# Kernel tuning notes

Measured on AMD Instinct MI355X. Metric: run time of the kernel, lower is better.

## Reference

```python
import jax, jax.numpy as jnp
import numpy as np

GRID_SIZE = 5
SPLINE_ORDER = 3
GRID_LO, GRID_HI = -1.0, 1.0
N_COEFF = GRID_SIZE + SPLINE_ORDER  # 8


def make_grid(in_features):
    # (in_features, grid_size + 2*spline_order + 1) = (in, 12)
    h = (GRID_HI - GRID_LO) / GRID_SIZE
    g = jnp.arange(-SPLINE_ORDER, GRID_SIZE + SPLINE_ORDER + 1, dtype=jnp.float32) * h + GRID_LO
    return jnp.broadcast_to(g, (in_features, g.shape[0]))


def b_splines(x, grid):
    # x: (N, in); grid: (in, G). Returns (N, in, grid_size+spline_order).
    xe = x[..., None]
    bases = ((xe >= grid[:, :-1]) & (xe < grid[:, 1:])).astype(x.dtype)
    for k in range(1, SPLINE_ORDER + 1):
        left = (xe - grid[:, :-(k + 1)]) / (grid[:, k:-1] - grid[:, :-(k + 1)]) * bases[..., :-1]
        right = (grid[:, k + 1:] - xe) / (grid[:, k + 1:] - grid[:, 1:-k]) * bases[..., 1:]
        bases = left + right
    return bases


def kan_linear(x, base_w, spline_w, scaler, grid):
    # base branch: SiLU(x) @ base_w^T
    base_out = jax.nn.silu(x) @ base_w.T
    # spline branch: basis (N,in,c) contracted with scaled spline weight (out,in,c)
    b = b_splines(x, grid)
    sw = spline_w * scaler[..., None]
    spline_out = jnp.einsum('nic,oic->no', b, sw)
    return base_out + spline_out


def setup_inputs() -> dict:
    key = jax.random.key(0)
    ks = jax.random.split(key, 7)
    d_model, d_hid = 512, 2049  # d_ff + 1
    s = 0.1  # keep activations roughly inside grid range
    return {
        "x": jax.random.normal(ks[0], (4096, d_model), dtype=jnp.float32) * 0.3,
        "base_w1": jax.random.normal(ks[1], (d_hid, d_model), dtype=jnp.float32) * s,
        "spline_w1": jax.random.normal(ks[2], (d_hid, d_model, N_COEFF), dtype=jnp.float32) * s,
        "scaler1": jax.random.normal(ks[3], (d_hid, d_model), dtype=jnp.float32) * s,
        "base_w2": jax.random.normal(ks[4], (d_model, d_hid), dtype=jnp.float32) * s,
        "spline_w2": jax.random.normal(ks[5], (d_model, d_hid, N_COEFF), dtype=jnp.float32) * s,
        "scaler2": jax.random.normal(ks[6], (d_model, d_hid), dtype=jnp.float32) * s,
    }


def reference(x, base_w1, spline_w1, scaler1, base_w2, spline_w2, scaler2):
    grid1 = make_grid(x.shape[-1])
    h = kan_linear(x, base_w1, spline_w1, scaler1, grid1)
    grid2 = make_grid(h.shape[-1])
    out = kan_linear(h, base_w2, spline_w2, scaler2, grid2)
    return out
```

## Files before the change

kernel.cpp:

```cpp
#include <hip/hip_runtime.h>
#include <hip/hip_bf16.h>

#define T_TOK 4096
#define I1    512
#define O1    2049
#define O1P   2176
#define K1    4608
#define NG1   576
#define I2    2049
#define O2    512
#define K2P   18496
#define NG2   2312
#define HLD   2176
#define SPLITS2 8
#define KLEN2 2368
#define NBY   32
#define PW1_NB 4896
#define E1_NB  9216
#define PW2_NB 8192

typedef __attribute__((ext_vector_type(8))) short short8;
typedef __attribute__((ext_vector_type(4))) float floatx4;
typedef __attribute__((address_space(3))) void* lds_ptr_t;
typedef const __attribute__((address_space(1))) void* gmem_ptr_t;

__device__ __forceinline__ unsigned short f2bf(float f) {
  union { __hip_bfloat16 h; unsigned short u; } cv;
  cv.h = __float2bfloat16(f);
  return cv.u;
}
__device__ __forceinline__ unsigned bfr(float f) {
  union { float f; unsigned u; } c; c.f = f;
  return (c.u + 0x8000u) >> 16;
}
__device__ __forceinline__ float silu_f(float x) { return x / (1.0f + __expf(-x)); }

__device__ __forceinline__ uint4 spline_pack(float h) {
  float u = (h + 2.2f) * 2.5f;
  int ji = (int)u;
  ji = ji < 0 ? 0 : (ji > 10 ? 10 : ji);
  float t = u - (float)ji;
  float it = 1.0f - t, t2 = t * t, t3 = t2 * t;
  float b0 = it * it * it * (1.0f / 6.0f);
  float b1 = (3.0f * t3 - 6.0f * t2 + 4.0f) * (1.0f / 6.0f);
  float b2 = (-3.0f * t3 + 3.0f * t2 + 3.0f * t + 1.0f) * (1.0f / 6.0f);
  float b3 = t3 * (1.0f / 6.0f);
  unsigned pk01 = bfr(b0) | (bfr(b1) << 16);
  unsigned pk23 = bfr(b2) | (bfr(b3) << 16);
  unsigned long long p64 = (unsigned long long)pk01 | ((unsigned long long)pk23 << 32);
  bool inR = (h >= -2.2f) && (h < 2.2f);
  p64 = inR ? p64 : 0ull;
  int sh = (ji - 3) * 16;
  int shr = sh < 0 ? -sh : 0;
  int shl = sh < 0 ? 0 : sh;
  __uint128_t v = ((__uint128_t)(p64 >> shr)) << shl;
  union { __uint128_t q; uint4 u4; } cv;
  cv.q = v;
  return cv.u4;
}

__global__ void prep1_kernel(const float* __restrict__ x, const float* __restrict__ bw1,
                             const float* __restrict__ sw1, const float* __restrict__ sc1,
                             unsigned short* __restrict__ A1, unsigned short* __restrict__ W1) {
  int b = blockIdx.x;
  union { unsigned short s[8]; uint4 v; } pk;
  if (b < PW1_NB) {
    int idx = b * 256 + threadIdx.x;
    int o = idx / NG1, g = idx - o * NG1;
    if (o >= O1) {
      pk.v = make_uint4(0u, 0u, 0u, 0u);
    } else if (g < 512) {
      const float4* p = (const float4*)&sw1[(size_t)o * 4096 + g * 8];
      float4 a = p[0], c = p[1];
      float sc = sc1[(size_t)o * I1 + g];
      pk.s[0] = f2bf(a.x * sc); pk.s[1] = f2bf(a.y * sc);
      pk.s[2] = f2bf(a.z * sc); pk.s[3] = f2bf(a.w * sc);
      pk.s[4] = f2bf(c.x * sc); pk.s[5] = f2bf(c.y * sc);
      pk.s[6] = f2bf(c.z * sc); pk.s[7] = f2bf(c.w * sc);
    } else {
      const float4* p = (const float4*)&bw1[(size_t)o * I1 + (g - 512) * 8];
      float4 a = p[0], c = p[1];
      pk.s[0] = f2bf(a.x); pk.s[1] = f2bf(a.y); pk.s[2] = f2bf(a.z); pk.s[3] = f2bf(a.w);
      pk.s[4] = f2bf(c.x); pk.s[5] = f2bf(c.y); pk.s[6] = f2bf(c.z); pk.s[7] = f2bf(c.w);
    }
    *(uint4*)&W1[(size_t)o * K1 + (size_t)g * 8] = pk.v;
  } else {
    int idx = (b - PW1_NB) * 256 + threadIdx.x;
    int m = idx / NG1, g = idx - m * NG1;
    if (g < 512) {
      pk.v = spline_pack(x[(size_t)m * I1 + g]);
    } else {
      const float4* p = (const float4*)&x[(size_t)m * I1 + (size_t)(g - 512) * 8];
      float4 a = p[0], c = p[1];
      pk.s[0] = f2bf(silu_f(a.x)); pk.s[1] = f2bf(silu_f(a.y));
      pk.s[2] = f2bf(silu_f(a.z)); pk.s[3] = f2bf(silu_f(a.w));
      pk.s[4] = f2bf(silu_f(c.x)); pk.s[5] = f2bf(silu_f(c.y));
      pk.s[6] = f2bf(silu_f(c.z)); pk.s[7] = f2bf(silu_f(c.w));
    }
    *(uint4*)&A1[(size_t)m * K1 + (size_t)g * 8] = pk.v;
  }
}

__global__ void pack_w2_kernel(const float* __restrict__ bw2, const float* __restrict__ sw2,
                               const float* __restrict__ sc2, unsigned short* __restrict__ W2) {
  int idx = blockIdx.x * 256 + threadIdx.x;
  int o = idx >> 12, g = idx & 4095;
  if (g >= NG2) return;
  union { unsigned short s[8]; uint4 v; } pk;
  if (g < 2049) {
    const float4* p = (const float4*)&sw2[(size_t)o * 16392 + (size_t)g * 8];
    float4 a = p[0], c = p[1];
    float sc = sc2[(size_t)o * I2 + g];
    pk.s[0] = f2bf(a.x * sc); pk.s[1] = f2bf(a.y * sc);
    pk.s[2] = f2bf(a.z * sc); pk.s[3] = f2bf(a.w * sc);
    pk.s[4] = f2bf(c.x * sc); pk.s[5] = f2bf(c.y * sc);
    pk.s[6] = f2bf(c.z * sc); pk.s[7] = f2bf(c.w * sc);
  } else if (g < 2306) {
    int c0 = (g - 2049) * 8;
#pragma unroll
    for (int j = 0; j < 8; ++j) {
      int k = c0 + j;
      pk.s[j] = (k < I2) ? f2bf(bw2[(size_t)o * I2 + k]) : (unsigned short)0;
    }
  } else {
    pk.v = make_uint4(0u, 0u, 0u, 0u);
  }
  *(uint4*)&W2[(size_t)o * K2P + (size_t)g * 8] = pk.v;
}

__global__ void expand2_kernel(const float* __restrict__ H, unsigned short* __restrict__ A) {
  int g = blockIdx.x * 256 + threadIdx.x;
  if (g >= NG2) return;
  int m = blockIdx.y;
  uint4 val;
  if (g < 2049) {
    val = spline_pack(H[(size_t)m * HLD + g]);
  } else if (g < 2306) {
    int c0 = (g - 2049) * 8;
    union { unsigned short s[8]; uint4 v; } pk;
#pragma unroll
    for (int c = 0; c < 8; ++c) {
      int idx = c0 + c;
      float v = 0.0f;
      if (idx < I2) v = silu_f(H[(size_t)m * HLD + idx]);
      pk.s[c] = f2bf(v);
    }
    val = pk.v;
  } else {
    val = make_uint4(0u, 0u, 0u, 0u);
  }
  *(uint4*)(A + (size_t)m * K2P + (size_t)g * 8) = val;
}

__global__ __launch_bounds__(256, 4)
void gemm_bt_kernel(const unsigned short* __restrict__ Aw, const unsigned short* __restrict__ Bw,
                    float* __restrict__ C, int Ktot, int N, int ldc, int kLen,
                    int nBx, int storeMode)
{
  __shared__ __align__(16) unsigned short As[128 * 64];
  __shared__ __align__(16) unsigned short Bs[128 * 64];

  const int Lb = blockIdx.x;
  const int m8 = Lb & 7;
  const int r  = Lb >> 3;
  const int bx = r % nBx;
  const int p  = m8 + ((r / nBx) << 3);
  const int by = p & (NBY - 1);
  const int bz = p >> 5;

  const int tid = threadIdx.x;
  const int ks = bz * kLen;
  int ke = ks + kLen; if (ke > Ktot) ke = Ktot;

  const int w = tid >> 6, L = tid & 63, q = L >> 4, ln = L & 15;
  const int wm = (w & 1) << 6, wn = (w >> 1) << 6;

  floatx4 zf = {0.f, 0.f, 0.f, 0.f};
  floatx4 acc[4][4];
#pragma unroll
  for (int mt = 0; mt < 4; ++mt)
#pragma unroll
    for (int nt = 0; nt < 4; ++nt)
      acc[mt][nt] = zf;

  const unsigned short* ga[4];
  const unsigned short* gb[4];
  int ldsOff[4];
#pragma unroll
  for (int r4 = 0; r4 < 4; ++r4) {
    int e = r4 * 256 + tid;
    int br = e >> 3;
    int cg = (e & 7) ^ (br & 7);
    ga[r4] = Aw + ((long)by * 128 + br) * (long)Ktot + ks + cg * 8;
    gb[r4] = Bw + ((long)bx * 128 + br) * (long)Ktot + ks + cg * 8;
    ldsOff[r4] = e * 8;
  }

  for (int kc = ks; kc < ke; kc += 64) {
    __syncthreads();
#pragma unroll
    for (int r4 = 0; r4 < 4; ++r4) {
      __builtin_amdgcn_global_load_lds((gmem_ptr_t)ga[r4], (lds_ptr_t)&As[ldsOff[r4]], 16, 0, 0);
      ga[r4] += 64;
      __builtin_amdgcn_global_load_lds((gmem_ptr_t)gb[r4], (lds_ptr_t)&Bs[ldsOff[r4]], 16, 0, 0);
      gb[r4] += 64;
    }
    __syncthreads();

#pragma unroll
    for (int s = 0; s < 2; ++s) {
      short8 af[4], bf[4];
#pragma unroll
      for (int mt = 0; mt < 4; ++mt) {
        int rr = wm + mt * 16 + ln;
        int cl = ((s << 2) | q) ^ (rr & 7);
        af[mt] = *(const short8*)&As[rr * 64 + cl * 8];
      }
#pragma unroll
      for (int nt = 0; nt < 4; ++nt) {
        int rr = wn + nt * 16 + ln;
        int cl = ((s << 2) | q) ^ (rr & 7);
        bf[nt] = *(const short8*)&Bs[rr * 64 + cl * 8];
      }
#pragma unroll
      for (int mt = 0; mt < 4; ++mt)
#pragma unroll
        for (int nt = 0; nt < 4; ++nt)
          acc[mt][nt] = __builtin_amdgcn_mfma_f32_16x16x32_bf16(af[mt], bf[nt], acc[mt][nt], 0, 0, 0);
    }
  }

  if (storeMode == 0) {
#pragma unroll
    for (int mt = 0; mt < 4; ++mt) {
#pragma unroll
      for (int nt = 0; nt < 4; ++nt) {
        int n = bx * 128 + wn + nt * 16 + ln;
        if (n < N) {
          int m0 = by * 128 + wm + mt * 16 + q * 4;
#pragma unroll
          for (int rg = 0; rg < 4; ++rg)
            C[(size_t)(m0 + rg) * ldc + n] = acc[mt][nt][rg];
        }
      }
    }
  } else {
#pragma unroll
    for (int mt = 0; mt < 4; ++mt) {
#pragma unroll
      for (int nt = 0; nt < 4; ++nt) {
        int n = bx * 128 + wn + nt * 16 + ln;
        if (n < N) {
          int m0 = by * 128 + wm + mt * 16 + q * 4;
#pragma unroll
          for (int rg = 0; rg < 4; ++rg)
            atomicAdd(&C[(size_t)(m0 + rg) * ldc + n], acc[mt][nt][rg]);
        }
      }
    }
  }
}

extern "C" void kernel_launch(void* const* d_in, const int* in_sizes, int n_in,
                              void* d_out, int out_size, void* d_ws, size_t ws_size,
                              hipStream_t stream) {
  const float* x   = (const float*)d_in[0];
  const float* bw1 = (const float*)d_in[1];
  const float* sw1 = (const float*)d_in[2];
  const float* sc1 = (const float*)d_in[3];
  const float* bw2 = (const float*)d_in[4];
  const float* sw2 = (const float*)d_in[5];
  const float* sc2 = (const float*)d_in[6];
  float* out = (float*)d_out;

  float* H = (float*)d_ws;
  unsigned short* A2 = (unsigned short*)(H + (size_t)T_TOK * HLD);
  unsigned short* A1 = A2 + (size_t)T_TOK * K2P;
  unsigned short* W1 = A1 + (size_t)T_TOK * K1;
  unsigned short* W2 = A1;

  hipMemsetAsync(d_out, 0, (size_t)out_size * sizeof(float), stream);

  prep1_kernel<<<PW1_NB + E1_NB, 256, 0, stream>>>(x, bw1, sw1, sc1, A1, W1);

  gemm_bt_kernel<<<(O1P / 128) * NBY, 256, 0, stream>>>(
      A1, W1, H, K1, O1, HLD, K1, O1P / 128, 0);

  pack_w2_kernel<<<PW2_NB, 256, 0, stream>>>(bw2, sw2, sc2, W2);

  expand2_kernel<<<dim3((NG2 + 255) / 256, T_TOK), 256, 0, stream>>>(H, A2);

  gemm_bt_kernel<<<(O2 / 128) * NBY * SPLITS2, 256, 0, stream>>>(
      A2, W2, out, K2P, O2, O2, KLEN2, O2 / 128, 2);
}
```

Baseline: 417.3 us.

## Replace GEMM with 256x128 triple-buffered pipelined kernel and split odd column to GEMV

Replaces the 128x128 double-sync GEMM with a 512-thread, 256x128-tile kernel that triple-buffers LDS, interleaves direct global-to-LDS prefetch with MFMA phases, and raises MFMA wave priority. The odd 2049th output column of layer 1 moves to a separate GEMV kernel so the main GEMM works on an aligned 2048-wide N with no padding tiles. The layer-2 split-K factor drops from 8 to 4, which halves the atomic traffic. The tradeoffs are higher LDS and register pressure, fewer workgroups in flight, and an extra kernel launch.

```diff
diff --git a/kernel.cpp b/kernel.cpp
--- a/kernel.cpp
+++ b/kernel.cpp
@@ -11,10 +11,9 @@
 #define O2    512
 #define K2P   18496
 #define NG2   2312
-#define HLD   2176
-#define SPLITS2 8
-#define KLEN2 2368
-#define NBY   32
+#define N1G   2048
+#define SPLITS2 4
+#define KLEN2 4672
 #define PW1_NB 4896
 #define E1_NB  9216
 #define PW2_NB 8192
@@ -28,6 +27,9 @@
   union { __hip_bfloat16 h; unsigned short u; } cv;
   cv.h = __float2bfloat16(f);
   return cv.u;
+}
+__device__ __forceinline__ float b2f(unsigned short u) {
+  union { float f; unsigned u; } c; c.u = (unsigned)u << 16; return c.f;
 }
 __device__ __forceinline__ unsigned bfr(float f) {
   union { float f; unsigned u; } c; c.f = f;
@@ -101,6 +103,28 @@
   }
 }
 
+__global__ void gemv_col_kernel(const unsigned short* __restrict__ A1,
+                                const unsigned short* __restrict__ W1,
+                                float* __restrict__ Hcol) {
+  int m = blockIdx.x * 4 + (threadIdx.x >> 6);
+  int lane = threadIdx.x & 63;
+  const unsigned short* a  = A1 + (size_t)m * K1;
+  const unsigned short* wr = W1 + (size_t)2048 * K1;
+  float s = 0.0f;
+#pragma unroll
+  for (int c = 0; c < 9; ++c) {
+    int off = (c * 64 + lane) * 8;
+    short8 av = *(const short8*)(a + off);
+    short8 wv = *(const short8*)(wr + off);
+#pragma unroll
+    for (int j = 0; j < 8; ++j)
+      s += b2f((unsigned short)av[j]) * b2f((unsigned short)wv[j]);
+  }
+#pragma unroll
+  for (int d = 32; d >= 1; d >>= 1) s += __shfl_down(s, d);
+  if (lane == 0) Hcol[m] = s;
+}
+
 __global__ void pack_w2_kernel(const float* __restrict__ bw2, const float* __restrict__ sw2,
                                const float* __restrict__ sc2, unsigned short* __restrict__ W2) {
   int idx = blockIdx.x * 256 + threadIdx.x;
@@ -128,13 +152,16 @@
   *(uint4*)&W2[(size_t)o * K2P + (size_t)g * 8] = pk.v;
 }
 
-__global__ void expand2_kernel(const float* __restrict__ H, unsigned short* __restrict__ A) {
+__global__ void expand2_kernel(const float* __restrict__ H, const float* __restrict__ Hcol,
+                               unsigned short* __restrict__ A) {
   int g = blockIdx.x * 256 + threadIdx.x;
   if (g >= NG2) return;
   int m = blockIdx.y;
+  float hc = Hcol[m];
   uint4 val;
   if (g < 2049) {
-    val = spline_pack(H[(size_t)m * HLD + g]);
+    float h = (g < N1G) ? H[(size_t)m * N1G + g] : hc;
+    val = spline_pack(h);
   } else if (g < 2306) {
     int c0 = (g - 2049) * 8;
     union { unsigned short s[8]; uint4 v; } pk;
@@ -142,7 +169,10 @@
     for (int c = 0; c < 8; ++c) {
       int idx = c0 + c;
       float v = 0.0f;
-      if (idx < I2) v = silu_f(H[(size_t)m * HLD + idx]);
+      if (idx < I2) {
+        float h = (idx < N1G) ? H[(size_t)m * N1G + idx] : hc;
+        v = silu_f(h);
+      }
       pk.s[c] = f2bf(v);
     }
     val = pk.v;
@@ -152,112 +182,181 @@
   *(uint4*)(A + (size_t)m * K2P + (size_t)g * 8) = val;
 }
 
-__global__ __launch_bounds__(256, 4)
-void gemm_bt_kernel(const unsigned short* __restrict__ Aw, const unsigned short* __restrict__ Bw,
-                    float* __restrict__ C, int Ktot, int N, int ldc, int kLen,
-                    int nBx, int storeMode)
+__global__ __launch_bounds__(512, 2)
+void gemm_rk3_kernel(const unsigned short* __restrict__ Aw, const unsigned short* __restrict__ Bw,
+                     float* __restrict__ C, int Ktot, int ldc, int kLen,
+                     int nBx, int nBy, int storeMode)
 {
-  __shared__ __align__(16) unsigned short As[128 * 64];
-  __shared__ __align__(16) unsigned short Bs[128 * 64];
+  __shared__ __align__(16) unsigned short As[3][16384];
+  __shared__ __align__(16) unsigned short Bs[3][8192];
 
   const int Lb = blockIdx.x;
-  const int m8 = Lb & 7;
-  const int r  = Lb >> 3;
-  const int bx = r % nBx;
-  const int p  = m8 + ((r / nBx) << 3);
-  const int by = p & (NBY - 1);
-  const int bz = p >> 5;
+  const int wgid = (Lb & 7) * 32 + (Lb >> 3);
+  const int bx = wgid % nBx;
+  const int tq = wgid / nBx;
+  const int by = tq % nBy;
+  const int bz = tq / nBy;
 
   const int tid = threadIdx.x;
   const int ks = bz * kLen;
   int ke = ks + kLen; if (ke > Ktot) ke = Ktot;
+  const int ntiles = (ke - ks) >> 6;
 
   const int w = tid >> 6, L = tid & 63, q = L >> 4, ln = L & 15;
-  const int wm = (w & 1) << 6, wn = (w >> 1) << 6;
+  const int wmh = w & 1;
+  const int wnq = w >> 1;
+  const int xb = ln & 7;
 
   floatx4 zf = {0.f, 0.f, 0.f, 0.f};
-  floatx4 acc[4][4];
-#pragma unroll
-  for (int mt = 0; mt < 4; ++mt)
-#pragma unroll
-    for (int nt = 0; nt < 4; ++nt)
-      acc[mt][nt] = zf;
-
-  const unsigned short* ga[4];
-  const unsigned short* gb[4];
-  int ldsOff[4];
-#pragma unroll
-  for (int r4 = 0; r4 < 4; ++r4) {
-    int e = r4 * 256 + tid;
-    int br = e >> 3;
-    int cg = (e & 7) ^ (br & 7);
-    ga[r4] = Aw + ((long)by * 128 + br) * (long)Ktot + ks + cg * 8;
-    gb[r4] = Bw + ((long)bx * 128 + br) * (long)Ktot + ks + cg * 8;
-    ldsOff[r4] = e * 8;
-  }
-
-  for (int kc = ks; kc < ke; kc += 64) {
-    __syncthreads();
-#pragma unroll
-    for (int r4 = 0; r4 < 4; ++r4) {
-      __builtin_amdgcn_global_load_lds((gmem_ptr_t)ga[r4], (lds_ptr_t)&As[ldsOff[r4]], 16, 0, 0);
-      ga[r4] += 64;
-      __builtin_amdgcn_global_load_lds((gmem_ptr_t)gb[r4], (lds_ptr_t)&Bs[ldsOff[r4]], 16, 0, 0);
-      gb[r4] += 64;
-    }
-    __syncthreads();
-
-#pragma unroll
-    for (int s = 0; s < 2; ++s) {
-      short8 af[4], bf[4];
-#pragma unroll
-      for (int mt = 0; mt < 4; ++mt) {
-        int rr = wm + mt * 16 + ln;
-        int cl = ((s << 2) | q) ^ (rr & 7);
-        af[mt] = *(const short8*)&As[rr * 64 + cl * 8];
-      }
-#pragma unroll
-      for (int nt = 0; nt < 4; ++nt) {
-        int rr = wn + nt * 16 + ln;
-        int cl = ((s << 2) | q) ^ (rr & 7);
-        bf[nt] = *(const short8*)&Bs[rr * 64 + cl * 8];
-      }
-#pragma unroll
-      for (int mt = 0; mt < 4; ++mt)
-#pragma unroll
-        for (int nt = 0; nt < 4; ++nt)
-          acc[mt][nt] = __builtin_amdgcn_mfma_f32_16x16x32_bf16(af[mt], bf[nt], acc[mt][nt], 0, 0, 0);
-    }
-  }
-
+  floatx4 acc[8][2];
+#pragma unroll
+  for (int f = 0; f < 8; ++f) { acc[f][0] = zf; acc[f][1] = zf; }
+
+  const unsigned short* gA[4];
+  const unsigned short* gB[2];
+  int loA[4], loB[2];
+#pragma unroll
+  for (int l = 0; l < 4; ++l) {
+    int e = l * 512 + tid;
+    int br = e >> 3, cg = (e & 7) ^ (br & 7);
+    gA[l] = Aw + (size_t)(by * 256 + br) * Ktot + ks + cg * 8;
+    loA[l] = e * 8;
+  }
+#pragma unroll
+  for (int l = 0; l < 2; ++l) {
+    int e = l * 512 + tid;
+    int br = e >> 3, cg = (e & 7) ^ (br & 7);
+    gB[l] = Bw + (size_t)(bx * 128 + br) * Ktot + ks + cg * 8;
+    loB[l] = e * 8;
+  }
+
+#pragma unroll
+  for (int tt = 0; tt < 2; ++tt) {
+#pragma unroll
+    for (int l = 0; l < 4; ++l)
+      __builtin_amdgcn_global_load_lds((gmem_ptr_t)(gA[l] + tt * 64), (lds_ptr_t)&As[tt][loA[l]], 16, 0, 0);
+#pragma unroll
+    for (int l = 0; l < 2; ++l)
+      __builtin_amdgcn_global_load_lds((gmem_ptr_t)(gB[l] + tt * 64), (lds_ptr_t)&Bs[tt][loB[l]], 16, 0, 0);
+  }
+#pragma unroll
+  for (int l = 0; l < 4; ++l) gA[l] += 128;
+#pragma unroll
+  for (int l = 0; l < 2; ++l) gB[l] += 128;
+  asm volatile("s_waitcnt vmcnt(6)" ::: "memory");
+  asm volatile("s_barrier" ::: "memory");
+
+  int cs = 0;
+  for (int t = 0; t < ntiles; ++t) {
+    int ss = cs + 2; if (ss >= 3) ss -= 3;
+    const unsigned short* Asp = &As[cs][0];
+    const unsigned short* Bsp = &Bs[cs][0];
+    const bool pf = (t + 2 < ntiles);
+    short8 af[4], bf[2];
+
+    {
+      const int cl = q ^ xb;
+      bf[0] = *(const short8*)&Bsp[(wnq * 32 + ln) * 64 + cl * 8];
+      bf[1] = *(const short8*)&Bsp[(wnq * 32 + 16 + ln) * 64 + cl * 8];
+#pragma unroll
+      for (int j = 0; j < 4; ++j)
+        af[j] = *(const short8*)&Asp[(wmh * 128 + j * 16 + ln) * 64 + cl * 8];
+      if (pf) {
+        __builtin_amdgcn_global_load_lds((gmem_ptr_t)gA[0], (lds_ptr_t)&As[ss][loA[0]], 16, 0, 0);
+        __builtin_amdgcn_global_load_lds((gmem_ptr_t)gA[1], (lds_ptr_t)&As[ss][loA[1]], 16, 0, 0);
+      }
+      asm volatile("s_barrier" ::: "memory");
+      __builtin_amdgcn_s_setprio(1);
+#pragma unroll
+      for (int j = 0; j < 4; ++j) {
+        acc[j][0] = __builtin_amdgcn_mfma_f32_16x16x32_bf16(af[j], bf[0], acc[j][0], 0, 0, 0);
+        acc[j][1] = __builtin_amdgcn_mfma_f32_16x16x32_bf16(af[j], bf[1], acc[j][1], 0, 0, 0);
+      }
+      __builtin_amdgcn_s_setprio(0);
+      asm volatile("s_barrier" ::: "memory");
+    }
+    {
+      const int cl = q ^ xb;
+#pragma unroll
+      for (int j = 0; j < 4; ++j)
+        af[j] = *(const short8*)&Asp[(wmh * 128 + (4 + j) * 16 + ln) * 64 + cl * 8];
+      if (pf) {
+        __builtin_amdgcn_global_load_lds((gmem_ptr_t)gA[2], (lds_ptr_t)&As[ss][loA[2]], 16, 0, 0);
+        __builtin_amdgcn_global_load_lds((gmem_ptr_t)gA[3], (lds_ptr_t)&As[ss][loA[3]], 16, 0, 0);
+      }
+      asm volatile("s_barrier" ::: "memory");
+      __builtin_amdgcn_s_setprio(1);
+#pragma unroll
+      for (int j = 0; j < 4; ++j) {
+        acc[4 + j][0] = __builtin_amdgcn_mfma_f32_16x16x32_bf16(af[j], bf[0], acc[4 + j][0], 0, 0, 0);
+        acc[4 + j][1] = __builtin_amdgcn_mfma_f32_16x16x32_bf16(af[j], bf[1], acc[4 + j][1], 0, 0, 0);
+      }
+      __builtin_amdgcn_s_setprio(0);
+      asm volatile("s_barrier" ::: "memory");
+    }
+    {
+      const int cl = (4 + q) ^ xb;
+      bf[0] = *(const short8*)&Bsp[(wnq * 32 + ln) * 64 + cl * 8];
+      bf[1] = *(const short8*)&Bsp[(wnq * 32 + 16 + ln) * 64 + cl * 8];
+#pragma unroll
+      for (int j = 0; j < 4; ++j)
+        af[j] = *(const short8*)&Asp[(wmh * 128 + j * 16 + ln) * 64 + cl * 8];
+      if (pf) {
+        __builtin_amdgcn_global_load_lds((gmem_ptr_t)gB[0], (lds_ptr_t)&Bs[ss][loB[0]], 16, 0, 0);
+        __builtin_amdgcn_global_load_lds((gmem_ptr_t)gB[1], (lds_ptr_t)&Bs[ss][loB[1]], 16, 0, 0);
+      }
+      asm volatile("s_barrier" ::: "memory");
+      __builtin_amdgcn_s_setprio(1);
+#pragma unroll
+      for (int j = 0; j < 4; ++j) {
+        acc[j][0] = __builtin_amdgcn_mfma_f32_16x16x32_bf16(af[j], bf[0], acc[j][0], 0, 0, 0);
+        acc[j][1] = __builtin_amdgcn_mfma_f32_16x16x32_bf16(af[j], bf[1], acc[j][1], 0, 0, 0);
+      }
+      __builtin_amdgcn_s_setprio(0);
+      asm volatile("s_barrier" ::: "memory");
+    }
+    {
+      const int cl = (4 + q) ^ xb;
+#pragma unroll
+      for (int j = 0; j < 4; ++j)
+        af[j] = *(const short8*)&Asp[(wmh * 128 + (4 + j) * 16 + ln) * 64 + cl * 8];
+      asm volatile("s_barrier" ::: "memory");
+      __builtin_amdgcn_s_setprio(1);
+#pragma unroll
+      for (int j = 0; j < 4; ++j) {
+        acc[4 + j][0] = __builtin_amdgcn_mfma_f32_16x16x32_bf16(af[j], bf[0], acc[4 + j][0], 0, 0, 0);
+        acc[4 + j][1] = __builtin_amdgcn_mfma_f32_16x16x32_bf16(af[j], bf[1], acc[4 + j][1], 0, 0, 0);
+      }
+      __builtin_amdgcn_s_setprio(0);
+      if (pf)                     asm volatile("s_waitcnt vmcnt(6)" ::: "memory");
+      else if (t + 1 < ntiles)    asm volatile("s_waitcnt vmcnt(0)" ::: "memory");
+      asm volatile("s_barrier" ::: "memory");
+    }
+#pragma unroll
+    for (int l = 0; l < 4; ++l) gA[l] += 64;
+#pragma unroll
+    for (int l = 0; l < 2; ++l) gB[l] += 64;
+    cs = cs + 1; if (cs >= 3) cs -= 3;
+  }
+
+  const int gm0 = by * 256 + wmh * 128 + q * 4;
+  const int gn0 = bx * 128 + wnq * 32 + ln;
   if (storeMode == 0) {
 #pragma unroll
-    for (int mt = 0; mt < 4; ++mt) {
-#pragma unroll
-      for (int nt = 0; nt < 4; ++nt) {
-        int n = bx * 128 + wn + nt * 16 + ln;
-        if (n < N) {
-          int m0 = by * 128 + wm + mt * 16 + q * 4;
-#pragma unroll
-          for (int rg = 0; rg < 4; ++rg)
-            C[(size_t)(m0 + rg) * ldc + n] = acc[mt][nt][rg];
-        }
-      }
-    }
+    for (int f = 0; f < 8; ++f)
+#pragma unroll
+      for (int n = 0; n < 2; ++n)
+#pragma unroll
+        for (int rg = 0; rg < 4; ++rg)
+          C[(size_t)(gm0 + f * 16 + rg) * ldc + (gn0 + n * 16)] = acc[f][n][rg];
   } else {
 #pragma unroll
-    for (int mt = 0; mt < 4; ++mt) {
-#pragma unroll
-      for (int nt = 0; nt < 4; ++nt) {
-        int n = bx * 128 + wn + nt * 16 + ln;
-        if (n < N) {
-          int m0 = by * 128 + wm + mt * 16 + q * 4;
-#pragma unroll
-          for (int rg = 0; rg < 4; ++rg)
-            atomicAdd(&C[(size_t)(m0 + rg) * ldc + n], acc[mt][nt][rg]);
-        }
-      }
-    }
+    for (int f = 0; f < 8; ++f)
+#pragma unroll
+      for (int n = 0; n < 2; ++n)
+#pragma unroll
+        for (int rg = 0; rg < 4; ++rg)
+          atomicAdd(&C[(size_t)(gm0 + f * 16 + rg) * ldc + (gn0 + n * 16)], acc[f][n][rg]);
   }
 }
 
@@ -274,7 +373,8 @@
   float* out = (float*)d_out;
 
   float* H = (float*)d_ws;
-  unsigned short* A2 = (unsigned short*)(H + (size_t)T_TOK * HLD);
+  float* Hcol = H + (size_t)T_TOK * N1G;
+  unsigned short* A2 = (unsigned short*)(Hcol + 4096);
   unsigned short* A1 = A2 + (size_t)T_TOK * K2P;
   unsigned short* W1 = A1 + (size_t)T_TOK * K1;
   unsigned short* W2 = A1;
@@ -283,13 +383,13 @@
 
   prep1_kernel<<<PW1_NB + E1_NB, 256, 0, stream>>>(x, bw1, sw1, sc1, A1, W1);
 
-  gemm_bt_kernel<<<(O1P / 128) * NBY, 256, 0, stream>>>(
-      A1, W1, H, K1, O1, HLD, K1, O1P / 128, 0);
+  gemm_rk3_kernel<<<256, 512, 0, stream>>>(A1, W1, H, K1, N1G, K1, 16, 16, 0);
+
+  gemv_col_kernel<<<T_TOK / 4, 256, 0, stream>>>(A1, W1, Hcol);
 
   pack_w2_kernel<<<PW2_NB, 256, 0, stream>>>(bw2, sw2, sc2, W2);
 
-  expand2_kernel<<<dim3((NG2 + 255) / 256, T_TOK), 256, 0, stream>>>(H, A2);
-
-  gemm_bt_kernel<<<(O2 / 128) * NBY * SPLITS2, 256, 0, stream>>>(
-      A2, W2, out, K2P, O2, O2, KLEN2, O2 / 128, 2);
-}
+  expand2_kernel<<<dim3((NG2 + 255) / 256, T_TOK), 256, 0, stream>>>(H, Hcol, A2);
+
+  gemm_rk3_kernel<<<256, 512, 0, stream>>>(A2, W2, out, K2P, O2, KLEN2, 4, 16, 1);
+}
```

Result: slower. 448.5 us (+7.5%).
